# Optimization experiments

Hardware: AMD Instinct MI355X
Metric: run time of the kernel (lower is better)

Reference implementation:

```python
import jax, jax.numpy as jnp
import numpy as np

N_NODES = 100000
N_EDGES = 1000000
D_IN = 64
D_OUT = 64
K_HOPS = 3


def setup_inputs() -> dict:
    key = jax.random.key(0)
    k1, k2, k3 = jax.random.split(key, 3)
    x = jax.random.normal(k1, (N_NODES, D_IN), dtype=jnp.float32)
    edge_index = jax.random.randint(k2, (2, N_EDGES), 0, N_NODES, dtype=jnp.int64)
    # Linear layer params (PyG Linear: y = x @ W.T + b)
    W = jax.random.normal(k3, (D_OUT, D_IN), dtype=jnp.float32) * (1.0 / np.sqrt(D_IN))
    b = jnp.zeros((D_OUT,), dtype=jnp.float32)
    return {"x": x, "edge_index": edge_index, "W": W, "b": b}


def reference(x, edge_index, W, b):
    # SGConv: x' = (D^{-1/2} (A + I) D^{-1/2})^K x, then Linear.
    N = x.shape[0]
    src, dst = edge_index[0], edge_index[1]
    loop = jnp.arange(N, dtype=edge_index.dtype)
    src = jnp.concatenate([src, loop])  # add self loops
    dst = jnp.concatenate([dst, loop])
    ones = jnp.ones(src.shape[0], dtype=x.dtype)
    deg = jax.ops.segment_sum(ones, dst, num_segments=N)  # in-degree incl. self loop
    dinv = jnp.where(deg > 0, jax.lax.rsqrt(deg), jnp.zeros_like(deg))
    norm = dinv[src] * dinv[dst]  # [E+N]
    for _ in range(K_HOPS):
        # out[dst] += norm * x[src]
        x = jax.ops.segment_sum(norm[:, None] * x[src], dst, num_segments=N)
    return x @ W.T + b
```

## Files before the change

### kernel.cpp

```cpp
#include <hip/hip_runtime.h>

#define NN 100000
#define NE 1000000
#define D  64
#define CAP 32
#define OVF_CAP 16384

#define FILL_EPT 8
#define FILL_CHUNK (256 * FILL_EPT)
#define FILL_NCHUNK ((NE + FILL_CHUNK - 1) / FILL_CHUNK)
#define PART_SZ 12500

__device__ __forceinline__ unsigned bf16rne(float f) {
    unsigned h = __float_as_uint(f);
    return (h + 0x7fffu + ((h >> 16) & 1u)) >> 16;
}
__device__ __forceinline__ uint2 pack4(float4 v) {
    uint2 o;
    o.x = bf16rne(v.x) | (bf16rne(v.y) << 16);
    o.y = bf16rne(v.z) | (bf16rne(v.w) << 16);
    return o;
}
__device__ __forceinline__ float4 unpack4(uint2 u) {
    float4 f;
    f.x = __uint_as_float(u.x << 16);
    f.y = __uint_as_float(u.x & 0xffff0000u);
    f.z = __uint_as_float(u.y << 16);
    f.w = __uint_as_float(u.y & 0xffff0000u);
    return f;
}

__global__ __launch_bounds__(256) void k_fill_bucket(const int* __restrict__ src,
                                                     const int* __restrict__ dst,
                                                     int* __restrict__ cnt,
                                                     int* __restrict__ bucket,
                                                     int* __restrict__ ovf_n,
                                                     int2* __restrict__ ovf) {
    const int part = blockIdx.x & 7;
    const int lo = part * PART_SZ, hi = lo + PART_SZ;
    const int base = (blockIdx.x >> 3) * FILL_CHUNK + threadIdx.x;
    #pragma unroll
    for (int it = 0; it < FILL_EPT; ++it) {
        int e = base + it * 256;
        if (e < NE) {
            int d = __builtin_nontemporal_load(&dst[e]);
            if (d >= lo && d < hi) {
                int s = __builtin_nontemporal_load(&src[e]);
                int c = atomicAdd(&cnt[d], 1);
                if (c < CAP) {
                    bucket[(size_t)d * CAP + c] = s;
                } else {
                    int i = atomicAdd(ovf_n, 1);
                    if (i < OVF_CAP) ovf[i] = make_int2(s, d);
                }
            }
        }
    }
}

__global__ __launch_bounds__(256) void k_cvt_linw(const float* __restrict__ x,
                                                  const float* __restrict__ W,
                                                  unsigned short* __restrict__ P) {
    const int lane = threadIdx.x & 63;
    const int wid  = (blockIdx.x * blockDim.x + threadIdx.x) >> 6;
    const int nw   = (gridDim.x * blockDim.x) >> 6;

    float w[64];
    const float4* W4 = (const float4*)W;
    #pragma unroll
    for (int i = 0; i < 16; ++i) {
        float4 q = W4[lane * 16 + i];
        w[4 * i + 0] = q.x; w[4 * i + 1] = q.y;
        w[4 * i + 2] = q.z; w[4 * i + 3] = q.w;
    }

    for (int n = wid; n < NN; n += nw) {
        float xl = __builtin_nontemporal_load(&x[(size_t)n * 64 + lane]);
        int xi = __float_as_int(xl);
        float y0 = 0.f, y1 = 0.f;
        #pragma unroll
        for (int i = 0; i < 64; i += 2) {
            y0 = fmaf(__int_as_float(__builtin_amdgcn_readlane(xi, i)),     w[i],     y0);
            y1 = fmaf(__int_as_float(__builtin_amdgcn_readlane(xi, i + 1)), w[i + 1], y1);
        }
        P[(size_t)n * 64 + lane] = (unsigned short)bf16rne(y0 + y1);
    }
}


template <bool F32OUT>
__device__ __forceinline__ void gather_body(const uint2* __restrict__ in2,
                                            const int* __restrict__ cnt,
                                            const int* __restrict__ bucket,
                                            const int* __restrict__ ovf_n,
                                            const int2* __restrict__ ovf,
                                            const float* __restrict__ bias,
                                            uint2* __restrict__ out2,
                                            float4* __restrict__ out4) {
    const int tid = threadIdx.x;
    const int l = tid & 15;
    const int n = blockIdx.x * 16 + (tid >> 4);

    const int cn = cnt[n];
    const int deg = min(cn, CAP);
    const float dn = rsqrtf((float)(cn + 1));

    float4 a0 = unpack4(in2[(size_t)n * 16 + l]);
    a0.x *= dn; a0.y *= dn; a0.z *= dn; a0.w *= dn;
    float4 a1 = make_float4(0.f, 0.f, 0.f, 0.f);
    float4 a2 = make_float4(0.f, 0.f, 0.f, 0.f);
    float4 a3 = make_float4(0.f, 0.f, 0.f, 0.f);

    if (deg > 0) {
        int   iA = (l < deg) ? l : 0;
        int   sA = bucket[(size_t)n * CAP + iA];
        float wA = rsqrtf((float)(cnt[sA] + 1));
        const int kmax = deg < 16 ? deg : 16;
        int k = 0;
        for (; k + 3 < kmax; k += 4) {
            int   s0 = __shfl(sA, k + 0, 16);
            int   s1 = __shfl(sA, k + 1, 16);
            int   s2 = __shfl(sA, k + 2, 16);
            int   s3 = __shfl(sA, k + 3, 16);
            float w0 = __shfl(wA, k + 0, 16);
            float w1 = __shfl(wA, k + 1, 16);
            float w2 = __shfl(wA, k + 2, 16);
            float w3 = __shfl(wA, k + 3, 16);
            float4 r0 = unpack4(in2[(size_t)s0 * 16 + l]);
            float4 r1 = unpack4(in2[(size_t)s1 * 16 + l]);
            float4 r2 = unpack4(in2[(size_t)s2 * 16 + l]);
            float4 r3 = unpack4(in2[(size_t)s3 * 16 + l]);
            a0.x = fmaf(w0, r0.x, a0.x); a0.y = fmaf(w0, r0.y, a0.y);
            a0.z = fmaf(w0, r0.z, a0.z); a0.w = fmaf(w0, r0.w, a0.w);
            a1.x = fmaf(w1, r1.x, a1.x); a1.y = fmaf(w1, r1.y, a1.y);
            a1.z = fmaf(w1, r1.z, a1.z); a1.w = fmaf(w1, r1.w, a1.w);
            a2.x = fmaf(w2, r2.x, a2.x); a2.y = fmaf(w2, r2.y, a2.y);
            a2.z = fmaf(w2, r2.z, a2.z); a2.w = fmaf(w2, r2.w, a2.w);
            a3.x = fmaf(w3, r3.x, a3.x); a3.y = fmaf(w3, r3.y, a3.y);
            a3.z = fmaf(w3, r3.z, a3.z); a3.w = fmaf(w3, r3.w, a3.w);
        }
        for (; k < kmax; ++k) {
            int   s0 = __shfl(sA, k, 16);
            float w0 = __shfl(wA, k, 16);
            float4 r0 = unpack4(in2[(size_t)s0 * 16 + l]);
            a0.x = fmaf(w0, r0.x, a0.x); a0.y = fmaf(w0, r0.y, a0.y);
            a0.z = fmaf(w0, r0.z, a0.z); a0.w = fmaf(w0, r0.w, a0.w);
        }
        if (deg > 16) {
            int   iB = (16 + l < deg) ? (16 + l) : 0;
            int   sB = bucket[(size_t)n * CAP + iB];
            float wB = rsqrtf((float)(cnt[sB] + 1));
            const int k2max = deg - 16;
            int k2 = 0;
            for (; k2 + 1 < k2max; k2 += 2) {
                int   s0 = __shfl(sB, k2 + 0, 16);
                int   s1 = __shfl(sB, k2 + 1, 16);
                float w0 = __shfl(wB, k2 + 0, 16);
                float w1 = __shfl(wB, k2 + 1, 16);
                float4 r0 = unpack4(in2[(size_t)s0 * 16 + l]);
                float4 r1 = unpack4(in2[(size_t)s1 * 16 + l]);
                a1.x = fmaf(w0, r0.x, a1.x); a1.y = fmaf(w0, r0.y, a1.y);
                a1.z = fmaf(w0, r0.z, a1.z); a1.w = fmaf(w0, r0.w, a1.w);
                a2.x = fmaf(w1, r1.x, a2.x); a2.y = fmaf(w1, r1.y, a2.y);
                a2.z = fmaf(w1, r1.z, a2.z); a2.w = fmaf(w1, r1.w, a2.w);
            }
            if (k2 < k2max) {
                int   s0 = __shfl(sB, k2, 16);
                float w0 = __shfl(wB, k2, 16);
                float4 r0 = unpack4(in2[(size_t)s0 * 16 + l]);
                a3.x = fmaf(w0, r0.x, a3.x); a3.y = fmaf(w0, r0.y, a3.y);
                a3.z = fmaf(w0, r0.z, a3.z); a3.w = fmaf(w0, r0.w, a3.w);
            }
        }
    }

    int m = *ovf_n;
    if (m > 0) {
        if (m > OVF_CAP) m = OVF_CAP;
        for (int i = 0; i < m; ++i) {
            int2 p = ovf[i];
            if (p.y == n) {
                float w = rsqrtf((float)(cnt[p.x] + 1));
                float4 r = unpack4(in2[(size_t)p.x * 16 + l]);
                a0.x = fmaf(w, r.x, a0.x); a0.y = fmaf(w, r.y, a0.y);
                a0.z = fmaf(w, r.z, a0.z); a0.w = fmaf(w, r.w, a0.w);
            }
        }
    }

    float4 r;
    r.x = dn * ((a0.x + a1.x) + (a2.x + a3.x));
    r.y = dn * ((a0.y + a1.y) + (a2.y + a3.y));
    r.z = dn * ((a0.z + a1.z) + (a2.z + a3.z));
    r.w = dn * ((a0.w + a1.w) + (a2.w + a3.w));
    if (F32OUT) {
        float4 bv = *(const float4*)&bias[4 * l];
        r.x += bv.x; r.y += bv.y; r.z += bv.z; r.w += bv.w;
        out4[(size_t)n * 16 + l] = r;
    } else {
        out2[(size_t)n * 16 + l] = pack4(r);
    }
}

__global__ __launch_bounds__(256) void k_gather_bf16(const uint2* __restrict__ in2,
                                                     const int* __restrict__ cnt,
                                                     const int* __restrict__ bucket,
                                                     const int* __restrict__ ovf_n,
                                                     const int2* __restrict__ ovf,
                                                     uint2* __restrict__ out2) {
    gather_body<false>(in2, cnt, bucket, ovf_n, ovf, nullptr, out2, nullptr);
}

__global__ __launch_bounds__(256) void k_gather_out(const uint2* __restrict__ in2,
                                                    const int* __restrict__ cnt,
                                                    const int* __restrict__ bucket,
                                                    const int* __restrict__ ovf_n,
                                                    const int2* __restrict__ ovf,
                                                    const float* __restrict__ bias,
                                                    float4* __restrict__ out4) {
    gather_body<true>(in2, cnt, bucket, ovf_n, ovf, bias, nullptr, out4);
}


__global__ void k_init_deg(float* __restrict__ deg) {
    int n = blockIdx.x * blockDim.x + threadIdx.x;
    if (n < NN) deg[n] = 1.0f;
}
__global__ void k_count_deg(const int* __restrict__ dst, float* __restrict__ deg) {
    int e = blockIdx.x * blockDim.x + threadIdx.x;
    if (e < NE) atomicAdd(&deg[dst[e]], 1.0f);
}
__global__ void k_dinv_f(float* __restrict__ deg) {
    int n = blockIdx.x * blockDim.x + threadIdx.x;
    if (n < NN) deg[n] = rsqrtf(deg[n]);
}
__global__ void k_prop_init(const float* __restrict__ in, const float* __restrict__ dinv,
                            float* __restrict__ out) {
    int i = blockIdx.x * blockDim.x + threadIdx.x;
    if (i < NN * D) {
        int n = i >> 6;
        float di = dinv[n];
        out[i] = di * di * in[i];
    }
}
__global__ __launch_bounds__(256) void k_prop_edges(const float* __restrict__ in,
                                                    const int* __restrict__ src,
                                                    const int* __restrict__ dst,
                                                    const float* __restrict__ dinv,
                                                    float* __restrict__ out) {
    int t = blockIdx.x * blockDim.x + threadIdx.x;
    int e = t >> 6, f = t & 63;
    if (e < NE) {
        int s = src[e], d = dst[e];
        float w = dinv[s] * dinv[d];
        atomicAdd(&out[d * D + f], w * in[s * D + f]);
    }
}
__global__ __launch_bounds__(256) void k_linear(const float* __restrict__ in,
                                                const float* __restrict__ W,
                                                const float* __restrict__ bias,
                                                float* __restrict__ out) {
    __shared__ float Wt[64 * 65];
    __shared__ float rows[4][64];
    const int tid = threadIdx.x;
    for (int m = tid; m < 64 * 64; m += 256) {
        int o = m >> 6, i = m & 63;
        Wt[i * 65 + o] = W[m];
    }
    __syncthreads();
    const int wave = tid >> 6, lane = tid & 63;
    const float bo = bias[lane];
    for (int base = blockIdx.x * 4; base < NN; base += gridDim.x * 4) {
        int n = base + wave;
        if (n < NN) {
            rows[wave][lane] = in[n * D + lane];
            float acc = bo;
            #pragma unroll
            for (int i = 0; i < 64; ++i)
                acc = fmaf(rows[wave][i], Wt[i * 65 + lane], acc);
            out[n * D + lane] = acc;
        }
    }
}


extern "C" void kernel_launch(void* const* d_in, const int* in_sizes, int n_in,
                              void* d_out, int out_size, void* d_ws, size_t ws_size,
                              hipStream_t stream) {
    const float* x   = (const float*)d_in[0];
    const int*   ei  = (const int*)d_in[1];
    const float* W   = (const float*)d_in[2];
    const float* b   = (const float*)d_in[3];
    float* out = (float*)d_out;

    const int* src = ei;
    const int* dst = ei + NE;

    char* ws = (char*)d_ws;
    size_t off = 0;
    auto take = [&](size_t bytes) -> char* {
        char* p = ws + off;
        off = (off + bytes + 255) & ~(size_t)255;
        return p;
    };

    int*            cnt    = (int*)take((size_t)NN * 4);
    int*            ovf_n  = (int*)take(256);
    float*          dinv   = (float*)take((size_t)NN * 4);
    int2*           ovf    = (int2*)take((size_t)OVF_CAP * 8);
    unsigned short* P      = (unsigned short*)take((size_t)NN * 64 * 2);
    unsigned short* Q      = (unsigned short*)take((size_t)NN * 64 * 2);
    int*            bucket = (int*)take((size_t)NN * CAP * 4);
    float*          buf    = (float*)P;
    const bool use_bucket = (off <= ws_size);

    const int B = 256;
    const int gridE1 = (NE + B - 1) / B;
    const int gridN1 = (NN + B - 1) / B;
    const int gridNW = NN / 16;

    if (use_bucket) {
        size_t zlen = (size_t)((char*)ovf_n - (char*)cnt) + 256;
        (void)hipMemsetAsync(cnt, 0, zlen, stream);
        k_fill_bucket<<<FILL_NCHUNK * 8, B, 0, stream>>>(src, dst, cnt, bucket, ovf_n, ovf);
        k_cvt_linw<<<2048, B, 0, stream>>>(x, W, P);
        k_gather_bf16<<<gridNW, B, 0, stream>>>((const uint2*)P, cnt, bucket, ovf_n, ovf, (uint2*)Q);
        k_gather_bf16<<<gridNW, B, 0, stream>>>((const uint2*)Q, cnt, bucket, ovf_n, ovf, (uint2*)P);
        k_gather_out<<<gridNW, B, 0, stream>>>((const uint2*)P, cnt, bucket, ovf_n, ovf, b, (float4*)out);
    } else {
        const int gridF = (NN * D + B - 1) / B;
        const int gridEW = (NE * 64) / B;
        k_init_deg <<<gridN1, B, 0, stream>>>(dinv);
        k_count_deg<<<gridE1, B, 0, stream>>>(dst, dinv);
        k_dinv_f   <<<gridN1, B, 0, stream>>>(dinv);
        k_prop_init <<<gridF, B, 0, stream>>>(x, dinv, buf);
        k_prop_edges<<<gridEW, B, 0, stream>>>(x, src, dst, dinv, buf);
        k_prop_init <<<gridF, B, 0, stream>>>(buf, dinv, out);
        k_prop_edges<<<gridEW, B, 0, stream>>>(buf, src, dst, dinv, out);
        k_prop_init <<<gridF, B, 0, stream>>>(out, dinv, buf);
        k_prop_edges<<<gridEW, B, 0, stream>>>(out, src, dst, dinv, buf);
        k_linear<<<NN / 4, B, 0, stream>>>(buf, W, b, out);
    }
}
```

Baseline: 172.0 us.

## Fuse bucket fill, projection and three gathers into one cooperative persistent kernel

```diff
diff --git a/kernel.cpp b/kernel.cpp
--- a/kernel.cpp
+++ b/kernel.cpp
@@ -1,4 +1,7 @@
 #include <hip/hip_runtime.h>
+#include <hip/hip_cooperative_groups.h>
+
+namespace cg = cooperative_groups;
 
 #define NN 100000
 #define NE 1000000
@@ -9,7 +12,10 @@
 #define FILL_EPT 8
 #define FILL_CHUNK (256 * FILL_EPT)
 #define FILL_NCHUNK ((NE + FILL_CHUNK - 1) / FILL_CHUNK)
+#define NFILL (FILL_NCHUNK * 8)
+#define NGAT (NN / 16)
 #define PART_SZ 12500
+#define MEGA_GRID 1024
 
 __device__ __forceinline__ unsigned bf16rne(float f) {
     unsigned h = __float_as_uint(f);
@@ -30,15 +36,14 @@
     return f;
 }
 
-__global__ __launch_bounds__(256) void k_fill_bucket(const int* __restrict__ src,
-                                                     const int* __restrict__ dst,
-                                                     int* __restrict__ cnt,
-                                                     int* __restrict__ bucket,
-                                                     int* __restrict__ ovf_n,
-                                                     int2* __restrict__ ovf) {
-    const int part = blockIdx.x & 7;
+
+__device__ __forceinline__ void fill_vb(int vb, const int* __restrict__ src,
+                                        const int* __restrict__ dst,
+                                        int* __restrict__ cnt, int* __restrict__ bucket,
+                                        int* __restrict__ ovf_n, int2* __restrict__ ovf) {
+    const int part = vb & 7;
     const int lo = part * PART_SZ, hi = lo + PART_SZ;
-    const int base = (blockIdx.x >> 3) * FILL_CHUNK + threadIdx.x;
+    const int base = (vb >> 3) * FILL_CHUNK + threadIdx.x;
     #pragma unroll
     for (int it = 0; it < FILL_EPT; ++it) {
         int e = base + it * 256;
@@ -58,13 +63,10 @@
     }
 }
 
-__global__ __launch_bounds__(256) void k_cvt_linw(const float* __restrict__ x,
-                                                  const float* __restrict__ W,
-                                                  unsigned short* __restrict__ P) {
+__device__ __forceinline__ void cvtlinw_body(int wid, int nw, const float* __restrict__ x,
+                                             const float* __restrict__ W,
+                                             unsigned short* __restrict__ P) {
     const int lane = threadIdx.x & 63;
-    const int wid  = (blockIdx.x * blockDim.x + threadIdx.x) >> 6;
-    const int nw   = (gridDim.x * blockDim.x) >> 6;
-
     float w[64];
     const float4* W4 = (const float4*)W;
     #pragma unroll
@@ -73,7 +75,6 @@
         w[4 * i + 0] = q.x; w[4 * i + 1] = q.y;
         w[4 * i + 2] = q.z; w[4 * i + 3] = q.w;
     }
-
     for (int n = wid; n < NN; n += nw) {
         float xl = __builtin_nontemporal_load(&x[(size_t)n * 64 + lane]);
         int xi = __float_as_int(xl);
@@ -87,19 +88,18 @@
     }
 }
 
-
 template <bool F32OUT>
-__device__ __forceinline__ void gather_body(const uint2* __restrict__ in2,
-                                            const int* __restrict__ cnt,
-                                            const int* __restrict__ bucket,
-                                            const int* __restrict__ ovf_n,
-                                            const int2* __restrict__ ovf,
-                                            const float* __restrict__ bias,
-                                            uint2* __restrict__ out2,
-                                            float4* __restrict__ out4) {
+__device__ __forceinline__ void gather_vb(int vb, const uint2* __restrict__ in2,
+                                          const int* __restrict__ cnt,
+                                          const int* __restrict__ bucket,
+                                          const int* __restrict__ ovf_n,
+                                          const int2* __restrict__ ovf,
+                                          const float* __restrict__ bias,
+                                          uint2* __restrict__ out2,
+                                          float4* __restrict__ out4) {
     const int tid = threadIdx.x;
     const int l = tid & 15;
-    const int n = blockIdx.x * 16 + (tid >> 4);
+    const int n = vb * 16 + (tid >> 4);
 
     const int cn = cnt[n];
     const int deg = min(cn, CAP);
@@ -202,13 +202,72 @@
     }
 }
 
+__global__ __launch_bounds__(256, 4) void k_mega(const float* __restrict__ x,
+                                                 const float* __restrict__ W,
+                                                 const float* __restrict__ bias,
+                                                 const int* __restrict__ src,
+                                                 const int* __restrict__ dst,
+                                                 int* __restrict__ cnt,
+                                                 int* __restrict__ bucket,
+                                                 int* __restrict__ ovf_n,
+                                                 int2* __restrict__ ovf,
+                                                 unsigned short* __restrict__ P,
+                                                 unsigned short* __restrict__ Q,
+                                                 float4* __restrict__ out) {
+    cg::grid_group g = cg::this_grid();
+    const int nb = gridDim.x;
+    const int bid = blockIdx.x;
+
+    for (int i = bid * 256 + threadIdx.x; i < NN; i += nb * 256) cnt[i] = 0;
+    if (bid == 0 && threadIdx.x == 0) *ovf_n = 0;
+    g.sync();
+
+    for (int vb = bid; vb < NFILL; vb += nb)
+        fill_vb(vb, src, dst, cnt, bucket, ovf_n, ovf);
+    {
+        int wid = (bid * 256 + threadIdx.x) >> 6;
+        int nw  = (nb * 256) >> 6;
+        cvtlinw_body(wid, nw, x, W, P);
+    }
+    g.sync();
+
+    for (int vb = bid; vb < NGAT; vb += nb)
+        gather_vb<false>(vb, (const uint2*)P, cnt, bucket, ovf_n, ovf, nullptr, (uint2*)Q, nullptr);
+    g.sync();
+
+    for (int vb = bid; vb < NGAT; vb += nb)
+        gather_vb<false>(vb, (const uint2*)Q, cnt, bucket, ovf_n, ovf, nullptr, (uint2*)P, nullptr);
+    g.sync();
+
+    for (int vb = bid; vb < NGAT; vb += nb)
+        gather_vb<true>(vb, (const uint2*)P, cnt, bucket, ovf_n, ovf, bias, nullptr, out);
+}
+
+
+__global__ __launch_bounds__(256) void k_fill_bucket(const int* __restrict__ src,
+                                                     const int* __restrict__ dst,
+                                                     int* __restrict__ cnt,
+                                                     int* __restrict__ bucket,
+                                                     int* __restrict__ ovf_n,
+                                                     int2* __restrict__ ovf) {
+    fill_vb(blockIdx.x, src, dst, cnt, bucket, ovf_n, ovf);
+}
+
+__global__ __launch_bounds__(256) void k_cvt_linw(const float* __restrict__ x,
+                                                  const float* __restrict__ W,
+                                                  unsigned short* __restrict__ P) {
+    int wid = (blockIdx.x * blockDim.x + threadIdx.x) >> 6;
+    int nw  = (gridDim.x * blockDim.x) >> 6;
+    cvtlinw_body(wid, nw, x, W, P);
+}
+
 __global__ __launch_bounds__(256) void k_gather_bf16(const uint2* __restrict__ in2,
                                                      const int* __restrict__ cnt,
                                                      const int* __restrict__ bucket,
                                                      const int* __restrict__ ovf_n,
                                                      const int2* __restrict__ ovf,
                                                      uint2* __restrict__ out2) {
-    gather_body<false>(in2, cnt, bucket, ovf_n, ovf, nullptr, out2, nullptr);
+    gather_vb<false>(blockIdx.x, in2, cnt, bucket, ovf_n, ovf, nullptr, out2, nullptr);
 }
 
 __global__ __launch_bounds__(256) void k_gather_out(const uint2* __restrict__ in2,
@@ -218,7 +277,7 @@
                                                     const int2* __restrict__ ovf,
                                                     const float* __restrict__ bias,
                                                     float4* __restrict__ out4) {
-    gather_body<true>(in2, cnt, bucket, ovf_n, ovf, bias, nullptr, out4);
+    gather_vb<true>(blockIdx.x, in2, cnt, bucket, ovf_n, ovf, bias, nullptr, out4);
 }
 
 
@@ -317,16 +376,25 @@
     const int B = 256;
     const int gridE1 = (NE + B - 1) / B;
     const int gridN1 = (NN + B - 1) / B;
-    const int gridNW = NN / 16;
 
     if (use_bucket) {
-        size_t zlen = (size_t)((char*)ovf_n - (char*)cnt) + 256;
-        (void)hipMemsetAsync(cnt, 0, zlen, stream);
-        k_fill_bucket<<<FILL_NCHUNK * 8, B, 0, stream>>>(src, dst, cnt, bucket, ovf_n, ovf);
-        k_cvt_linw<<<2048, B, 0, stream>>>(x, W, P);
-        k_gather_bf16<<<gridNW, B, 0, stream>>>((const uint2*)P, cnt, bucket, ovf_n, ovf, (uint2*)Q);
-        k_gather_bf16<<<gridNW, B, 0, stream>>>((const uint2*)Q, cnt, bucket, ovf_n, ovf, (uint2*)P);
-        k_gather_out<<<gridNW, B, 0, stream>>>((const uint2*)P, cnt, bucket, ovf_n, ovf, b, (float4*)out);
+        const float* xa = x; const float* Wa = W; const float* ba = b;
+        const int* sa = src; const int* da = dst;
+        int* ca = cnt; int* bu = bucket; int* on = ovf_n; int2* ov = ovf;
+        unsigned short* Pa = P; unsigned short* Qa = Q;
+        float4* oa = (float4*)out;
+        void* args[] = {&xa, &Wa, &ba, &sa, &da, &ca, &bu, &on, &ov, &Pa, &Qa, &oa};
+        hipError_t err = hipLaunchCooperativeKernel((const void*)k_mega, dim3(MEGA_GRID),
+                                                    dim3(B), args, 0, stream);
+        if (err != hipSuccess) {
+            size_t zlen = (size_t)((char*)ovf_n - (char*)cnt) + 256;
+            (void)hipMemsetAsync(cnt, 0, zlen, stream);
+            k_fill_bucket<<<NFILL, B, 0, stream>>>(src, dst, cnt, bucket, ovf_n, ovf);
+            k_cvt_linw<<<2048, B, 0, stream>>>(x, W, P);
+            k_gather_bf16<<<NGAT, B, 0, stream>>>((const uint2*)P, cnt, bucket, ovf_n, ovf, (uint2*)Q);
+            k_gather_bf16<<<NGAT, B, 0, stream>>>((const uint2*)Q, cnt, bucket, ovf_n, ovf, (uint2*)P);
+            k_gather_out<<<NGAT, B, 0, stream>>>((const uint2*)P, cnt, bucket, ovf_n, ovf, b, (float4*)out);
+        }
     } else {
         const int gridF = (NN * D + B - 1) / B;
         const int gridEW = (NE * 64) / B;
```

Measured after the change: 602.4 us. 3.5x slower.
